# Optimization experiments

Measured on AMD Instinct MI355X. Metric: run time of the kernel, lower is better.

The kernel has to match this reference:

```python
import jax, jax.numpy as jnp
import numpy as np

N_NODES = 100000
N_EDGES = 1600000
NODE_IN = 6
EDGE_IN = 4
HID = 128


def _glorot(key, shape):
    fan_in, fan_out = shape[0], shape[1]
    lim = (6.0 / (fan_in + fan_out)) ** 0.5
    return jax.random.uniform(key, shape, jnp.float32, -lim, lim)


def setup_inputs() -> dict:
    key = jax.random.key(0)
    ks = jax.random.split(key, 16)
    x = jax.random.normal(ks[0], (N_NODES, NODE_IN), jnp.float32)
    edge_index = jax.random.randint(ks[1], (2, N_EDGES), 0, N_NODES, jnp.int64)
    edge_attr = jax.random.normal(ks[2], (N_EDGES, EDGE_IN), jnp.float32)
    # SAGEConv params: out = x @ W_root + mean_neigh @ W_neigh + b
    params = {
        "w1_root": _glorot(ks[3], (NODE_IN, HID)),
        "w1_neigh": _glorot(ks[4], (NODE_IN, HID)),
        "b1": jnp.zeros((HID,), jnp.float32),
        "w2_root": _glorot(ks[5], (HID, HID)),
        "w2_neigh": _glorot(ks[6], (HID, HID)),
        "b2": jnp.zeros((HID,), jnp.float32),
        "w_e1": _glorot(ks[7], (2 * HID + EDGE_IN, HID)),
        "b_e1": jnp.zeros((HID,), jnp.float32),
        "w_e2": _glorot(ks[8], (HID, HID // 2)),
        "b_e2": jnp.zeros((HID // 2,), jnp.float32),
        "w_e3": _glorot(ks[9], (HID // 2, 1)),
        "b_e3": jnp.zeros((1,), jnp.float32),
    }
    return {"x": x, "edge_index": edge_index, "edge_attr": edge_attr, **params}


def _sage(x, src, dst, w_root, w_neigh, b):
    # mean aggregation of source features into destination nodes
    agg = jax.ops.segment_sum(x[src], dst, num_segments=N_NODES)
    cnt = jax.ops.segment_sum(jnp.ones((src.shape[0], 1), x.dtype), dst, num_segments=N_NODES)
    mean = agg / jnp.maximum(cnt, 1.0)
    return x @ w_root + mean @ w_neigh + b


def reference(x, edge_index, edge_attr,
              w1_root, w1_neigh, b1, w2_root, w2_neigh, b2,
              w_e1, b_e1, w_e2, b_e2, w_e3, b_e3):
    src, dst = edge_index[0], edge_index[1]
    h = jax.nn.relu(_sage(x, src, dst, w1_root, w1_neigh, b1))
    # dropout is identity in eval mode
    h = jax.nn.relu(_sage(h, src, dst, w2_root, w2_neigh, b2))
    # per-edge representation: [h[src], h[dst], edge_attr] -> MLP -> scalar
    e = jnp.concatenate([h[src], h[dst], edge_attr], axis=-1)  # [E, 2H+Ein]
    e = jax.nn.relu(e @ w_e1 + b_e1)
    e = jax.nn.relu(e @ w_e2 + b_e2)
    out = (e @ w_e3 + b_e3).squeeze(-1)  # [E]
    return out
```

## Files before the change

### kernel.cpp

```cpp
#include <hip/hip_runtime.h>
#include <hip/hip_bf16.h>
#include <stdint.h>


typedef unsigned short u16;
typedef short bf16x8 __attribute__((ext_vector_type(8)));
typedef float f32x4 __attribute__((ext_vector_type(4)));
typedef float f32x2 __attribute__((ext_vector_type(2)));

#define NMASK 0x1FFFF

__device__ __forceinline__ u16 f2b(float f) {
  unsigned u = __builtin_bit_cast(unsigned, f);
  u = u + 0x7fffu + ((u >> 16) & 1u);
  return (u16)(u >> 16);
}
__device__ __forceinline__ float bflo(unsigned u) {
  return __builtin_bit_cast(float, u << 16);
}
__device__ __forceinline__ float bfhi(unsigned u) {
  return __builtin_bit_cast(float, u & 0xffff0000u);
}
__device__ __forceinline__ f32x2 unpk2(unsigned u) {
  return (f32x2){bflo(u), bfhi(u)};
}
__device__ __forceinline__ unsigned pack2bf(float a, float b) {
  unsigned ua = __builtin_bit_cast(unsigned, a);
  unsigned ub = __builtin_bit_cast(unsigned, b);
  ua = ua + 0x7fffu + ((ua >> 16) & 1u);
  ub = ub + 0x7fffu + ((ub >> 16) & 1u);
  return (ua >> 16) | (ub & 0xffff0000u);
}
__device__ __forceinline__ unsigned packrn(f32x2 f) {
  __hip_bfloat162 h = __float22bfloat162_rn(make_float2(f.x, f.y));
  unsigned r;
  __builtin_memcpy(&r, &h, 4);
  return r;
}

__global__ void hist_kernel(const int* __restrict__ ei, int* __restrict__ cnt,
                            int E) {
  int e = blockIdx.x * blockDim.x + threadIdx.x;
  if (e < E) atomicAdd(&cnt[ei[E + e]], 1);
}

__global__ void scan_block_sums(const int* __restrict__ cnt,
                                int* __restrict__ partial, int N) {
  __shared__ int red[256];
  int t = threadIdx.x;
  int n = blockIdx.x * 256 + t;
  red[t] = (n < N) ? cnt[n] : 0;
  __syncthreads();
  for (int off = 128; off; off >>= 1) {
    if (t < off) red[t] += red[t + off];
    __syncthreads();
  }
  if (t == 0) partial[blockIdx.x] = red[0];
}

__global__ void scan_partials(int* __restrict__ partial,
                              int* __restrict__ rowptr, int NBLK, int E,
                              int N) {
  __shared__ int sc[512];
  int t = threadIdx.x;
  int v = (t < NBLK) ? partial[t] : 0;
  sc[t] = v;
  __syncthreads();
  for (int off = 1; off < 512; off <<= 1) {
    int a = (t >= off) ? sc[t - off] : 0;
    __syncthreads();
    sc[t] += a;
    __syncthreads();
  }
  if (t < NBLK) partial[t] = sc[t] - v;
  if (t == 0) rowptr[N] = E;
}

__global__ void scan_final(const int* __restrict__ partial,
                           int* __restrict__ cursor, int* __restrict__ rowptr,
                           int N) {
  __shared__ int sc[256];
  int t = threadIdx.x;
  int n = blockIdx.x * 256 + t;
  int v = (n < N) ? cursor[n] : 0;
  sc[t] = v;
  __syncthreads();
  for (int off = 1; off < 256; off <<= 1) {
    int a = (t >= off) ? sc[t - off] : 0;
    __syncthreads();
    sc[t] += a;
    __syncthreads();
  }
  int excl = partial[blockIdx.x] + sc[t] - v;
  if (n < N) {
    rowptr[n] = excl;
    cursor[n] = excl;
  }
}

__global__ void scatter_csr(const int* __restrict__ ei,
                            const float* __restrict__ attr,
                            int* __restrict__ cursor, uint2* __restrict__ csr2,
                            float4* __restrict__ attrp, int E) {
  int e = blockIdx.x * blockDim.x + threadIdx.x;
  if (e >= E) return;
  int s = ei[e];
  int d = ei[E + e];
  float4 a4 = *(const float4*)(attr + (size_t)e * 4);
  int pos = atomicAdd(&cursor[d], 1);
  unsigned long long v = (unsigned long long)(unsigned)s |
                         ((unsigned long long)(unsigned)d << 17) |
                         ((unsigned long long)(unsigned)e << 34);
  csr2[pos] = make_uint2((unsigned)v, (unsigned)(v >> 32));
  attrp[pos] = a4;
}

__global__ void pack_weights(const float* __restrict__ w2_root,
                             const float* __restrict__ w2_neigh,
                             const float* __restrict__ w_e1,
                             const float* __restrict__ w_e2,
                             const float* __restrict__ b_e1,
                             u16* __restrict__ B2f, u16* __restrict__ WSDf,
                             u16* __restrict__ W2f, float* __restrict__ pbias) {
  int t = blockIdx.x * 256 + threadIdx.x;
  if (t < 32768) {
    int j = t & 7, lane = (t >> 3) & 63, nt = (t >> 9) & 7, kt = t >> 12;
    int k = kt * 32 + (lane >> 4) * 8 + j;
    int n = nt * 16 + (lane & 15);
    float v = (k < 128) ? w2_root[k * 128 + n] : w2_neigh[(k - 128) * 128 + n];
    B2f[t] = f2b(v);
  } else if (t < 65536) {
    int t2 = t - 32768;
    int j = t2 & 7, lane = (t2 >> 3) & 63, nt = (t2 >> 9) & 15, kt = t2 >> 13;
    int k = kt * 32 + (lane >> 4) * 8 + j;
    int n = nt * 16 + (lane & 15);
    float v = (n < 128) ? w_e1[k * 128 + n] : w_e1[(128 + k) * 128 + (n - 128)];
    WSDf[t2] = f2b(v);
  } else if (t < 73728) {
    int t2 = t - 65536;
    int j = t2 & 7, lane = (t2 >> 3) & 63, nt = (t2 >> 9) & 3, kt = t2 >> 11;
    int k = kt * 32 + (lane >> 4) * 8 + j;
    int n = nt * 16 + (lane & 15);
    W2f[t2] = f2b(w_e2[k * 64 + n]);
  } else if (t < 73984) {
    int n = t - 73728;
    pbias[n] = (n < 128) ? 0.0f : b_e1[n - 128];
  }
}

__global__ __launch_bounds__(256) void agg1_kernel(
    const float* __restrict__ x, const int* __restrict__ rowptr,
    const uint2* __restrict__ csr2, float* __restrict__ mean1, int N) {
  int n = blockIdx.x * 4 + (threadIdx.x >> 6);
  if (n >= N) return;
  int lane = threadIdx.x & 63;
  int g = lane >> 3;
  int c = lane & 7;
  int beg = rowptr[n], end = rowptr[n + 1];
  float a = 0.0f;
  if (c < 6) {
    int idx[4];
#pragma unroll
    for (int j = 0; j < 4; j++) {
      int ii = beg + g + j * 8;
      idx[j] = (ii < end) ? (int)(csr2[ii].x & NMASK) : -1;
    }
    float v[4];
#pragma unroll
    for (int j = 0; j < 4; j++)
      v[j] = x[(size_t)(idx[j] < 0 ? 0 : idx[j]) * 6 + c];
#pragma unroll
    for (int j = 0; j < 4; j++)
      if (idx[j] >= 0) a += v[j];
    for (int ii = beg + g + 32; ii < end; ii += 8) {
      int s = (int)(csr2[ii].x & NMASK);
      a += x[(size_t)s * 6 + c];
    }
  }
  a += __shfl_xor(a, 8, 64);
  a += __shfl_xor(a, 16, 64);
  a += __shfl_xor(a, 32, 64);
  if (g == 0 && c < 6)
    mean1[(size_t)n * 6 + c] = a / (float)max(end - beg, 1);
}

__global__ __launch_bounds__(256) void dense1_kernel(
    const float* __restrict__ x, const float* __restrict__ mean1,
    const float* __restrict__ w_root, const float* __restrict__ w_neigh,
    const float* __restrict__ b, u16* __restrict__ cat2b, int N) {
  __shared__ float sxm[384];
  int t = threadIdx.x;
  int col = t & 127;
  int half = t >> 7;
  float wr[6], wn[6];
#pragma unroll
  for (int j = 0; j < 6; j++) {
    wr[j] = w_root[j * 128 + col];
    wn[j] = w_neigh[j * 128 + col];
  }
  float bb = b[col];
  for (int base = blockIdx.x * 32; base < N; base += gridDim.x * 32) {
    int cnt = min(32, N - base) * 6;
    __syncthreads();
    for (int i = t; i < 384; i += 256) {
      if (i < 192)
        sxm[i] = (i < cnt) ? x[(size_t)base * 6 + i] : 0.0f;
      else
        sxm[i] = (i - 192 < cnt) ? mean1[(size_t)base * 6 + (i - 192)] : 0.0f;
    }
    __syncthreads();
#pragma unroll
    for (int sub = 0; sub < 16; sub++) {
      int nl = sub * 2 + half;
      int n = base + nl;
      if (n < N) {
        float s = bb;
#pragma unroll
        for (int j = 0; j < 6; j++)
          s += sxm[nl * 6 + j] * wr[j] + sxm[192 + nl * 6 + j] * wn[j];
        cat2b[(size_t)n * 256 + col] = f2b(fmaxf(s, 0.0f));
      }
    }
  }
}

__global__ __launch_bounds__(256) void agg2_kernel(
    const u16* __restrict__ cat2b, u16* __restrict__ cat2w,
    const int* __restrict__ rowptr, const uint2* __restrict__ csr2, int N) {
  int n = blockIdx.x * 4 + (threadIdx.x >> 6);
  if (n >= N) return;
  int lane = threadIdx.x & 63;
  int g = lane >> 4;
  int c = lane & 15;
  int beg = rowptr[n], end = rowptr[n + 1];
  f32x2 acc2[4];
#pragma unroll
  for (int j = 0; j < 4; j++) acc2[j] = (f32x2){0.f, 0.f};

  const int DEPTH = 6;
  int idx[DEPTH];
#pragma unroll
  for (int j = 0; j < DEPTH; j++) {
    int ii = beg + g + j * 4;
    idx[j] = (ii < end) ? (int)(csr2[ii].x & NMASK) : -1;
  }
  uint4 u[DEPTH];
#pragma unroll
  for (int j = 0; j < DEPTH; j++) {
    int s = idx[j] < 0 ? 0 : idx[j];
    u[j] = *(const uint4*)(cat2b + (size_t)s * 256 + c * 8);
  }
#pragma unroll
  for (int j = 0; j < DEPTH; j++) {
    if (idx[j] >= 0) {
      acc2[0] += unpk2(u[j].x);
      acc2[1] += unpk2(u[j].y);
      acc2[2] += unpk2(u[j].z);
      acc2[3] += unpk2(u[j].w);
    }
  }
  for (int ii = beg + g + DEPTH * 4; ii < end; ii += 4) {
    int s = (int)(csr2[ii].x & NMASK);
    uint4 uu = *(const uint4*)(cat2b + (size_t)s * 256 + c * 8);
    acc2[0] += unpk2(uu.x);
    acc2[1] += unpk2(uu.y);
    acc2[2] += unpk2(uu.z);
    acc2[3] += unpk2(uu.w);
  }
#pragma unroll
  for (int j = 0; j < 4; j++) {
    acc2[j].x += __shfl_xor(acc2[j].x, 16, 64);
    acc2[j].y += __shfl_xor(acc2[j].y, 16, 64);
    acc2[j].x += __shfl_xor(acc2[j].x, 32, 64);
    acc2[j].y += __shfl_xor(acc2[j].y, 32, 64);
  }
  if (g == 0) {
    float inv = 1.0f / (float)max(end - beg, 1);
    uint4 ov;
    ov.x = packrn(acc2[0] * inv);
    ov.y = packrn(acc2[1] * inv);
    ov.z = packrn(acc2[2] * inv);
    ov.w = packrn(acc2[3] * inv);
    *(uint4*)(cat2w + (size_t)n * 256 + 128 + c * 8) = ov;
  }
}

template <int KT, int NT, bool RELU>
__global__ __launch_bounds__(256) void mfma_gemm(
    const u16* __restrict__ A, int lda, const u16* __restrict__ Bf,
    const float* __restrict__ bias, u16* __restrict__ C, int ldc, int M) {
  __shared__ u16 sB[KT * NT * 512];
  int tid = threadIdx.x;
  for (int i = tid; i < KT * NT * 64; i += 256)
    ((uint4*)sB)[i] = ((const uint4*)Bf)[i];
  int w = tid >> 6, l = tid & 63;
  int quad = l >> 4, col16 = l & 15;
  int rowA = blockIdx.x * 64 + w * 16 + col16;
  bool rv = rowA < M;
  const u16* ap = A + (size_t)rowA * lda + quad * 8;
  f32x4 acc[NT];
#pragma unroll
  for (int nt = 0; nt < NT; nt++) acc[nt] = (f32x4){0.f, 0.f, 0.f, 0.f};
  __syncthreads();
#pragma unroll
  for (int kt = 0; kt < KT; kt++) {
    bf16x8 av = {};
    if (rv) av = *(const bf16x8*)(ap + kt * 32);
#pragma unroll
    for (int nt = 0; nt < NT; nt++) {
      bf16x8 bv = *(const bf16x8*)(sB + ((kt * NT + nt) * 64 + l) * 8);
      acc[nt] = __builtin_amdgcn_mfma_f32_16x16x32_bf16(av, bv, acc[nt], 0, 0, 0);
    }
  }
  int rowbase = blockIdx.x * 64 + w * 16 + quad * 4;
#pragma unroll
  for (int r = 0; r < 4; r++) {
    int row = rowbase + r;
    if (row < M) {
#pragma unroll
      for (int nt = 0; nt < NT; nt++) {
        float v = acc[nt][r] + bias[nt * 16 + col16];
        if (RELU) v = fmaxf(v, 0.0f);
        C[(size_t)row * ldc + nt * 16 + col16] = f2b(v);
      }
    }
  }
}

__global__ __launch_bounds__(256) void edge_mfma_kernel(
    const u16* __restrict__ Pcatb, const uint2* __restrict__ csr2,
    const float4* __restrict__ attrp, const float* __restrict__ w_e1,
    const u16* __restrict__ W2f, const float* __restrict__ b_e2,
    const float* __restrict__ w_e3, const float* __restrict__ b_e3,
    float* __restrict__ out, int E) {
  __shared__ u16 sV[64 * 136];
  __shared__ u16 sW2[8192];

  int tid = threadIdx.x;
  int w = tid >> 6, l = tid & 63, quad = l >> 4, c16 = l & 15;
  int egrp = tid >> 4, ac16 = tid & 15;

  for (int i = tid; i < 1024; i += 256)
    ((uint4*)sW2)[i] = ((const uint4*)W2f)[i];

  f32x2 wa2[4][4];
#pragma unroll
  for (int j = 0; j < 4; j++) {
    float4 w0 = *(const float4*)(w_e1 + (256 + j) * 128 + ac16 * 8);
    float4 w1 = *(const float4*)(w_e1 + (256 + j) * 128 + ac16 * 8 + 4);
    wa2[j][0] = (f32x2){w0.x, w0.y};
    wa2[j][1] = (f32x2){w0.z, w0.w};
    wa2[j][2] = (f32x2){w1.x, w1.y};
    wa2[j][3] = (f32x2){w1.z, w1.w};
  }
  float w3v[4], be2[4];
#pragma unroll
  for (int nt = 0; nt < 4; nt++) {
    w3v[nt] = w_e3[nt * 16 + c16];
    be2[nt] = b_e2[nt * 16 + c16];
  }
  float b3 = b_e3[0];

  int tiles = (E + 63) >> 6;
  int S = gridDim.x;

  uint2 pk[4];
  uint4 ps[4], pd[4];
  float4 at[4];
  int eidr[4];

  auto load_pk = [&](int t) {
#pragma unroll
    for (int it = 0; it < 4; it++) {
      int e = min(t * 64 + it * 16 + egrp, E - 1);
      pk[it] = csr2[e];
    }
  };
  auto issue_gather = [&](int t) {
#pragma unroll
    for (int it = 0; it < 4; it++) {
      unsigned long long v = ((unsigned long long)pk[it].y << 32) | pk[it].x;
      int s = (int)(v & NMASK);
      int d = (int)((v >> 17) & NMASK);
      eidr[it] = (int)(v >> 34);
      ps[it] = *(const uint4*)(Pcatb + (size_t)s * 256 + ac16 * 8);
      pd[it] = *(const uint4*)(Pcatb + (size_t)d * 256 + 128 + ac16 * 8);
      int e = min(t * 64 + it * 16 + egrp, E - 1);
      at[it] = attrp[e];
    }
  };

  int t = blockIdx.x;
  if (t < tiles) {
    load_pk(t);
    issue_gather(t);
    if (t + S < tiles) load_pk(t + S);
  }
  for (; t < tiles; t += S) {
#pragma unroll
    for (int it = 0; it < 4; it++) {
      int e = it * 16 + egrp;
      uint4 psu = ps[it], pdu = pd[it];
      float4 a4 = at[it];
      unsigned pu[4] = {psu.x, psu.y, psu.z, psu.w};
      unsigned du[4] = {pdu.x, pdu.y, pdu.z, pdu.w};
      uint4 ov;
      unsigned* op = (unsigned*)&ov;
#pragma unroll
      for (int p2 = 0; p2 < 4; p2++) {
        f32x2 f = unpk2(pu[p2]) + unpk2(du[p2]);
        f += a4.x * wa2[0][p2];
        f += a4.y * wa2[1][p2];
        f += a4.z * wa2[2][p2];
        f += a4.w * wa2[3][p2];
        f = __builtin_elementwise_max(f, (f32x2){0.f, 0.f});
        op[p2] = packrn(f);
      }
      *(uint4*)(sV + e * 136 + ac16 * 8) = ov;
      if (ac16 == 0) *(unsigned*)(sV + e * 136 + 128) = (unsigned)eidr[it];
    }
    if (t + S < tiles) {
      issue_gather(t + S);
      if (t + 2 * S < tiles) load_pk(t + 2 * S);
    }
    __syncthreads();
    f32x4 acc[4];
#pragma unroll
    for (int nt = 0; nt < 4; nt++) acc[nt] = (f32x4){0.f, 0.f, 0.f, 0.f};
    const u16* vp = sV + (w * 16 + c16) * 136 + quad * 8;
#pragma unroll
    for (int kt = 0; kt < 4; kt++) {
      bf16x8 av = *(const bf16x8*)(vp + kt * 32);
#pragma unroll
      for (int nt = 0; nt < 4; nt++) {
        bf16x8 bv = *(const bf16x8*)(sW2 + ((kt * 4 + nt) * 64 + l) * 8);
        acc[nt] = __builtin_amdgcn_mfma_f32_16x16x32_bf16(av, bv, acc[nt], 0, 0, 0);
      }
    }
#pragma unroll
    for (int r = 0; r < 4; r++) {
      float p = 0.0f;
#pragma unroll
      for (int nt = 0; nt < 4; nt++)
        p += fmaxf(acc[nt][r] + be2[nt], 0.0f) * w3v[nt];
      p += __shfl_xor(p, 1, 64);
      p += __shfl_xor(p, 2, 64);
      p += __shfl_xor(p, 4, 64);
      p += __shfl_xor(p, 8, 64);
      if (c16 == 0) {
        int eloc = w * 16 + quad * 4 + r;
        if (t * 64 + eloc < E) {
          unsigned eid = *(const unsigned*)(sV + eloc * 136 + 128);
          out[eid] = p + b3;
        }
      }
    }
    __syncthreads();
  }
}

extern "C" void kernel_launch(void* const* d_in, const int* in_sizes, int n_in,
                              void* d_out, int out_size, void* d_ws,
                              size_t ws_size, hipStream_t stream) {
  const float* x        = (const float*)d_in[0];
  const int*   ei       = (const int*)d_in[1];
  const float* attr     = (const float*)d_in[2];
  const float* w1_root  = (const float*)d_in[3];
  const float* w1_neigh = (const float*)d_in[4];
  const float* b1       = (const float*)d_in[5];
  const float* w2_root  = (const float*)d_in[6];
  const float* w2_neigh = (const float*)d_in[7];
  const float* b2       = (const float*)d_in[8];
  const float* w_e1     = (const float*)d_in[9];
  const float* b_e1     = (const float*)d_in[10];
  const float* w_e2     = (const float*)d_in[11];
  const float* b_e2     = (const float*)d_in[12];
  const float* w_e3     = (const float*)d_in[13];
  const float* b_e3     = (const float*)d_in[14];
  float* out = (float*)d_out;

  int N = in_sizes[0] / 6;
  int E = in_sizes[2] / 4;
  int NBLK = (N + 255) / 256;

  int* wsi = (int*)d_ws;
  int*    rowptr  = wsi;
  int*    cursor  = wsi + 100004;
  int*    partial = wsi + 200004;
  uint2*  csr2    = (uint2*)(wsi + 200520);
  float*  mean1   = (float*)(wsi + 3400520);
  u16*    cat2b   = (u16*)(wsi + 4000520);
  u16*    h2b     = (u16*)(wsi + 16800520);
  u16*    B2f     = (u16*)(wsi + 23200520);
  u16*    WSDf    = (u16*)(wsi + 23216904);
  u16*    W2f     = (u16*)(wsi + 23233288);
  float*  pbias   = (float*)(wsi + 23237384);
  float4* attrp   = (float4*)(wsi + 23237640);

  (void)hipMemsetAsync(cursor, 0, (size_t)N * sizeof(int), stream);

  pack_weights<<<289, 256, 0, stream>>>(w2_root, w2_neigh, w_e1, w_e2, b_e1,
                                        B2f, WSDf, W2f, pbias);

  hist_kernel<<<(E + 255) / 256, 256, 0, stream>>>(ei, cursor, E);
  scan_block_sums<<<NBLK, 256, 0, stream>>>(cursor, partial, N);
  scan_partials<<<1, 512, 0, stream>>>(partial, rowptr, NBLK, E, N);
  scan_final<<<NBLK, 256, 0, stream>>>(partial, cursor, rowptr, N);
  scatter_csr<<<(E + 255) / 256, 256, 0, stream>>>(ei, attr, cursor, csr2,
                                                   attrp, E);

  agg1_kernel<<<(N + 3) / 4, 256, 0, stream>>>(x, rowptr, csr2, mean1, N);
  dense1_kernel<<<1024, 256, 0, stream>>>(x, mean1, w1_root, w1_neigh, b1,
                                          cat2b, N);

  agg2_kernel<<<(N + 3) / 4, 256, 0, stream>>>(cat2b, cat2b, rowptr, csr2, N);

  int gblocks = (N + 63) / 64;
  mfma_gemm<8, 8, true><<<gblocks, 256, 0, stream>>>(cat2b, 256, B2f, b2, h2b,
                                                     128, N);
  mfma_gemm<4, 16, false><<<gblocks, 256, 0, stream>>>(h2b, 128, WSDf, pbias,
                                                       cat2b, 256, N);

  edge_mfma_kernel<<<1024, 256, 0, stream>>>(cat2b, csr2, attrp, w_e1, W2f,
                                             b_e2, w_e3, b_e3, out, E);
}
```

Baseline: 604.0 us.

## Pack edge records with bf16 attrs and add compact source index array

The scatter step now writes a 16-byte per-edge record (src, dst, edge id, bf16-packed edge attributes) plus a separate 4-byte source index array. The aggregation kernels read the compact src array and the edge MLP kernel reads one record per edge instead of separate csr and float4 attribute streams, which cuts memory traffic. The agg2 prefetch depth is raised and the node GEMMs switch to 512-thread blocks covering 128 rows. Edge attributes are rounded to bf16, which adds a small precision loss.

```diff
diff --git a/kernel.cpp b/kernel.cpp
--- a/kernel.cpp
+++ b/kernel.cpp
@@ -98,21 +98,23 @@
   }
 }
 
-__global__ void scatter_csr(const int* __restrict__ ei,
+__global__ void scatter_rec(const int* __restrict__ ei,
                             const float* __restrict__ attr,
-                            int* __restrict__ cursor, uint2* __restrict__ csr2,
-                            float4* __restrict__ attrp, int E) {
+                            int* __restrict__ cursor, uint4* __restrict__ rec,
+                            unsigned* __restrict__ src4, int E) {
   int e = blockIdx.x * blockDim.x + threadIdx.x;
   if (e >= E) return;
   int s = ei[e];
   int d = ei[E + e];
   float4 a4 = *(const float4*)(attr + (size_t)e * 4);
   int pos = atomicAdd(&cursor[d], 1);
-  unsigned long long v = (unsigned long long)(unsigned)s |
-                         ((unsigned long long)(unsigned)d << 17) |
-                         ((unsigned long long)(unsigned)e << 34);
-  csr2[pos] = make_uint2((unsigned)v, (unsigned)(v >> 32));
-  attrp[pos] = a4;
+  uint4 r;
+  r.x = (unsigned)s | ((unsigned)(d & 0x7FFF) << 17);
+  r.y = ((unsigned)d >> 15) | ((unsigned)e << 2);
+  r.z = pack2bf(a4.x, a4.y);
+  r.w = pack2bf(a4.z, a4.w);
+  rec[pos] = r;
+  src4[pos] = (unsigned)s;
 }
 
 __global__ void pack_weights(const float* __restrict__ w2_root,
@@ -150,7 +152,7 @@
 
 __global__ __launch_bounds__(256) void agg1_kernel(
     const float* __restrict__ x, const int* __restrict__ rowptr,
-    const uint2* __restrict__ csr2, float* __restrict__ mean1, int N) {
+    const unsigned* __restrict__ src4, float* __restrict__ mean1, int N) {
   int n = blockIdx.x * 4 + (threadIdx.x >> 6);
   if (n >= N) return;
   int lane = threadIdx.x & 63;
@@ -163,7 +165,7 @@
 #pragma unroll
     for (int j = 0; j < 4; j++) {
       int ii = beg + g + j * 8;
-      idx[j] = (ii < end) ? (int)(csr2[ii].x & NMASK) : -1;
+      idx[j] = (ii < end) ? (int)src4[ii] : -1;
     }
     float v[4];
 #pragma unroll
@@ -173,8 +175,7 @@
     for (int j = 0; j < 4; j++)
       if (idx[j] >= 0) a += v[j];
     for (int ii = beg + g + 32; ii < end; ii += 8) {
-      int s = (int)(csr2[ii].x & NMASK);
-      a += x[(size_t)s * 6 + c];
+      a += x[(size_t)src4[ii] * 6 + c];
     }
   }
   a += __shfl_xor(a, 8, 64);
@@ -226,7 +227,7 @@
 
 __global__ __launch_bounds__(256) void agg2_kernel(
     const u16* __restrict__ cat2b, u16* __restrict__ cat2w,
-    const int* __restrict__ rowptr, const uint2* __restrict__ csr2, int N) {
+    const int* __restrict__ rowptr, const unsigned* __restrict__ src4, int N) {
   int n = blockIdx.x * 4 + (threadIdx.x >> 6);
   if (n >= N) return;
   int lane = threadIdx.x & 63;
@@ -237,12 +238,12 @@
 #pragma unroll
   for (int j = 0; j < 4; j++) acc2[j] = (f32x2){0.f, 0.f};
 
-  const int DEPTH = 6;
+  const int DEPTH = 8;
   int idx[DEPTH];
 #pragma unroll
   for (int j = 0; j < DEPTH; j++) {
     int ii = beg + g + j * 4;
-    idx[j] = (ii < end) ? (int)(csr2[ii].x & NMASK) : -1;
+    idx[j] = (ii < end) ? (int)src4[ii] : -1;
   }
   uint4 u[DEPTH];
 #pragma unroll
@@ -260,8 +261,7 @@
     }
   }
   for (int ii = beg + g + DEPTH * 4; ii < end; ii += 4) {
-    int s = (int)(csr2[ii].x & NMASK);
-    uint4 uu = *(const uint4*)(cat2b + (size_t)s * 256 + c * 8);
+    uint4 uu = *(const uint4*)(cat2b + (size_t)src4[ii] * 256 + c * 8);
     acc2[0] += unpk2(uu.x);
     acc2[1] += unpk2(uu.y);
     acc2[2] += unpk2(uu.z);
@@ -286,16 +286,16 @@
 }
 
 template <int KT, int NT, bool RELU>
-__global__ __launch_bounds__(256) void mfma_gemm(
+__global__ __launch_bounds__(512) void mfma_gemm(
     const u16* __restrict__ A, int lda, const u16* __restrict__ Bf,
     const float* __restrict__ bias, u16* __restrict__ C, int ldc, int M) {
   __shared__ u16 sB[KT * NT * 512];
   int tid = threadIdx.x;
-  for (int i = tid; i < KT * NT * 64; i += 256)
+  for (int i = tid; i < KT * NT * 64; i += 512)
     ((uint4*)sB)[i] = ((const uint4*)Bf)[i];
   int w = tid >> 6, l = tid & 63;
   int quad = l >> 4, col16 = l & 15;
-  int rowA = blockIdx.x * 64 + w * 16 + col16;
+  int rowA = blockIdx.x * 128 + w * 16 + col16;
   bool rv = rowA < M;
   const u16* ap = A + (size_t)rowA * lda + quad * 8;
   f32x4 acc[NT];
@@ -312,7 +312,7 @@
       acc[nt] = __builtin_amdgcn_mfma_f32_16x16x32_bf16(av, bv, acc[nt], 0, 0, 0);
     }
   }
-  int rowbase = blockIdx.x * 64 + w * 16 + quad * 4;
+  int rowbase = blockIdx.x * 128 + w * 16 + quad * 4;
 #pragma unroll
   for (int r = 0; r < 4; r++) {
     int row = rowbase + r;
@@ -328,11 +328,10 @@
 }
 
 __global__ __launch_bounds__(256) void edge_mfma_kernel(
-    const u16* __restrict__ Pcatb, const uint2* __restrict__ csr2,
-    const float4* __restrict__ attrp, const float* __restrict__ w_e1,
+    const u16* __restrict__ Pcatb, const uint4* __restrict__ rec,
     const u16* __restrict__ W2f, const float* __restrict__ b_e2,
     const float* __restrict__ w_e3, const float* __restrict__ b_e3,
-    float* __restrict__ out, int E) {
+    const float* __restrict__ w_e1, float* __restrict__ out, int E) {
   __shared__ u16 sV[64 * 136];
   __shared__ u16 sW2[8192];
 
@@ -364,44 +363,48 @@
   int tiles = (E + 63) >> 6;
   int S = gridDim.x;
 
-  uint2 pk[4];
+  uint4 rc[4];
   uint4 ps[4], pd[4];
-  float4 at[4];
   int eidr[4];
 
-  auto load_pk = [&](int t) {
+  auto load_rec = [&](int t) {
 #pragma unroll
     for (int it = 0; it < 4; it++) {
       int e = min(t * 64 + it * 16 + egrp, E - 1);
-      pk[it] = csr2[e];
+      rc[it] = rec[e];
     }
   };
-  auto issue_gather = [&](int t) {
+  auto issue_gather = [&]() {
 #pragma unroll
     for (int it = 0; it < 4; it++) {
-      unsigned long long v = ((unsigned long long)pk[it].y << 32) | pk[it].x;
-      int s = (int)(v & NMASK);
-      int d = (int)((v >> 17) & NMASK);
-      eidr[it] = (int)(v >> 34);
+      int s = (int)(rc[it].x & NMASK);
+      int d = (int)(((rc[it].x >> 17) | (rc[it].y << 15)) & NMASK);
+      eidr[it] = (int)(rc[it].y >> 2);
       ps[it] = *(const uint4*)(Pcatb + (size_t)s * 256 + ac16 * 8);
       pd[it] = *(const uint4*)(Pcatb + (size_t)d * 256 + 128 + ac16 * 8);
-      int e = min(t * 64 + it * 16 + egrp, E - 1);
-      at[it] = attrp[e];
     }
   };
 
   int t = blockIdx.x;
+  uint4 rcn[4];
   if (t < tiles) {
-    load_pk(t);
-    issue_gather(t);
-    if (t + S < tiles) load_pk(t + S);
+    load_rec(t);
+    issue_gather();
+    if (t + S < tiles) {
+#pragma unroll
+      for (int it = 0; it < 4; it++) {
+        int e = min((t + S) * 64 + it * 16 + egrp, E - 1);
+        rcn[it] = rec[e];
+      }
+    }
   }
   for (; t < tiles; t += S) {
 #pragma unroll
     for (int it = 0; it < 4; it++) {
       int e = it * 16 + egrp;
       uint4 psu = ps[it], pdu = pd[it];
-      float4 a4 = at[it];
+      f32x2 a01 = unpk2(rc[it].z);
+      f32x2 a23 = unpk2(rc[it].w);
       unsigned pu[4] = {psu.x, psu.y, psu.z, psu.w};
       unsigned du[4] = {pdu.x, pdu.y, pdu.z, pdu.w};
       uint4 ov;
@@ -409,10 +412,10 @@
 #pragma unroll
       for (int p2 = 0; p2 < 4; p2++) {
         f32x2 f = unpk2(pu[p2]) + unpk2(du[p2]);
-        f += a4.x * wa2[0][p2];
-        f += a4.y * wa2[1][p2];
-        f += a4.z * wa2[2][p2];
-        f += a4.w * wa2[3][p2];
+        f += a01.x * wa2[0][p2];
+        f += a01.y * wa2[1][p2];
+        f += a23.x * wa2[2][p2];
+        f += a23.y * wa2[3][p2];
         f = __builtin_elementwise_max(f, (f32x2){0.f, 0.f});
         op[p2] = packrn(f);
       }
@@ -420,8 +423,16 @@
       if (ac16 == 0) *(unsigned*)(sV + e * 136 + 128) = (unsigned)eidr[it];
     }
     if (t + S < tiles) {
-      issue_gather(t + S);
-      if (t + 2 * S < tiles) load_pk(t + 2 * S);
+#pragma unroll
+      for (int it = 0; it < 4; it++) rc[it] = rcn[it];
+      issue_gather();
+      if (t + 2 * S < tiles) {
+#pragma unroll
+        for (int it = 0; it < 4; it++) {
+          int e = min((t + 2 * S) * 64 + it * 16 + egrp, E - 1);
+          rcn[it] = rec[e];
+        }
+      }
     }
     __syncthreads();
     f32x4 acc[4];
@@ -484,18 +495,18 @@
   int NBLK = (N + 255) / 256;
 
   int* wsi = (int*)d_ws;
-  int*    rowptr  = wsi;
-  int*    cursor  = wsi + 100004;
-  int*    partial = wsi + 200004;
-  uint2*  csr2    = (uint2*)(wsi + 200520);
-  float*  mean1   = (float*)(wsi + 3400520);
-  u16*    cat2b   = (u16*)(wsi + 4000520);
-  u16*    h2b     = (u16*)(wsi + 16800520);
-  u16*    B2f     = (u16*)(wsi + 23200520);
-  u16*    WSDf    = (u16*)(wsi + 23216904);
-  u16*    W2f     = (u16*)(wsi + 23233288);
-  float*  pbias   = (float*)(wsi + 23237384);
-  float4* attrp   = (float4*)(wsi + 23237640);
+  int*      rowptr  = wsi;
+  int*      cursor  = wsi + 100004;
+  int*      partial = wsi + 200004;
+  unsigned* src4    = (unsigned*)(wsi + 200516);
+  uint4*    rec     = (uint4*)(wsi + 1800520);
+  float*    mean1   = (float*)(wsi + 8200520);
+  u16*      cat2b   = (u16*)(wsi + 8800520);
+  u16*      h2b     = (u16*)(wsi + 21600520);
+  u16*      B2f     = (u16*)(wsi + 28000520);
+  u16*      WSDf    = (u16*)(wsi + 28016904);
+  u16*      W2f     = (u16*)(wsi + 28033288);
+  float*    pbias   = (float*)(wsi + 28037384);
 
   (void)hipMemsetAsync(cursor, 0, (size_t)N * sizeof(int), stream);
 
@@ -506,21 +517,21 @@
   scan_block_sums<<<NBLK, 256, 0, stream>>>(cursor, partial, N);
   scan_partials<<<1, 512, 0, stream>>>(partial, rowptr, NBLK, E, N);
   scan_final<<<NBLK, 256, 0, stream>>>(partial, cursor, rowptr, N);
-  scatter_csr<<<(E + 255) / 256, 256, 0, stream>>>(ei, attr, cursor, csr2,
-                                                   attrp, E);
-
-  agg1_kernel<<<(N + 3) / 4, 256, 0, stream>>>(x, rowptr, csr2, mean1, N);
+  scatter_rec<<<(E + 255) / 256, 256, 0, stream>>>(ei, attr, cursor, rec,
+                                                   src4, E);
+
+  agg1_kernel<<<(N + 3) / 4, 256, 0, stream>>>(x, rowptr, src4, mean1, N);
   dense1_kernel<<<1024, 256, 0, stream>>>(x, mean1, w1_root, w1_neigh, b1,
                                           cat2b, N);
 
-  agg2_kernel<<<(N + 3) / 4, 256, 0, stream>>>(cat2b, cat2b, rowptr, csr2, N);
-
-  int gblocks = (N + 63) / 64;
-  mfma_gemm<8, 8, true><<<gblocks, 256, 0, stream>>>(cat2b, 256, B2f, b2, h2b,
+  agg2_kernel<<<(N + 3) / 4, 256, 0, stream>>>(cat2b, cat2b, rowptr, src4, N);
+
+  int gblocks = (N + 127) / 128;
+  mfma_gemm<8, 8, true><<<gblocks, 512, 0, stream>>>(cat2b, 256, B2f, b2, h2b,
                                                      128, N);
-  mfma_gemm<4, 16, false><<<gblocks, 256, 0, stream>>>(h2b, 128, WSDf, pbias,
+  mfma_gemm<4, 16, false><<<gblocks, 512, 0, stream>>>(h2b, 128, WSDf, pbias,
                                                        cat2b, 256, N);
 
-  edge_mfma_kernel<<<1024, 256, 0, stream>>>(cat2b, csr2, attrp, w_e1, W2f,
-                                             b_e2, w_e3, b_e3, out, E);
-}
+  edge_mfma_kernel<<<1024, 256, 0, stream>>>(cat2b, rec, W2f, b_e2, w_e3,
+                                             b_e3, w_e1, out, E);
+}
```

Result: no change. 595.9 us (-1.4%).
